# Performance work log

Hardware: AMD Instinct MI355X
Metric: run time of the kernel (lower is better)

The kernel has to match this reference:

```python
import jax, jax.numpy as jnp
import numpy as np


def conv1x1(x, w, b):
    # x: [B,C,H,W], w: [O,C], b: [O]
    return jnp.einsum('bchw,oc->bohw', x, w) + b[None, :, None, None]


def resize_bilinear(x, h, w):
    # matches torch F.interpolate(mode='bilinear', align_corners=False), no antialias
    B, C = x.shape[:2]
    return jax.image.resize(x, (B, C, h, w), method='bilinear', antialias=False)


def attend(q_map, k_map, v_map, num_heads, scale):
    # q_map/k_map/v_map: [B, hidden, H, W] -> out [B, hidden, H, W]
    B, D, H, W = q_map.shape
    hd = D // num_heads
    N = H * W
    q = q_map.reshape(B, num_heads, hd, N).transpose(0, 1, 3, 2)  # [B,h,N,d]
    k = k_map.reshape(B, num_heads, hd, N)                         # [B,h,d,N]
    v = v_map.reshape(B, num_heads, hd, N).transpose(0, 1, 3, 2)  # [B,h,N,d]
    scores = jnp.einsum('bhnd,bhdm->bhnm', q, k) * scale
    attn = jax.nn.softmax(scores, axis=-1)
    out = jnp.einsum('bhnm,bhmd->bhnd', attn, v)                   # [B,h,N,d]
    return out.transpose(0, 1, 3, 2).reshape(B, D, H, W)


NUM_HEADS = 8
HIDDEN = 256
HEAD_DIM = HIDDEN // NUM_HEADS
SCALE = HEAD_DIM ** -0.5


def setup_inputs() -> dict:
    key = jax.random.key(0)
    ks = jax.random.split(key, 20)
    C_h, C_l = 128, 256
    inp = {
        'high_feat': jax.random.normal(ks[0], (2, C_h, 64, 64), jnp.float32),
        'low_feat': jax.random.normal(ks[1], (2, C_l, 32, 32), jnp.float32),
    }
    def lin(k, o, c):
        kw, kb = jax.random.split(k)
        s = 1.0 / np.sqrt(c)
        return (jax.random.uniform(kw, (o, c), jnp.float32, -s, s),
                jax.random.uniform(kb, (o,), jnp.float32, -s, s))
    inp['q_high_w'], inp['q_high_b'] = lin(ks[2], HIDDEN, C_h)
    inp['k_high_w'], inp['k_high_b'] = lin(ks[3], HIDDEN, C_h)
    inp['v_high_w'], inp['v_high_b'] = lin(ks[4], HIDDEN, C_h)
    inp['q_low_w'], inp['q_low_b'] = lin(ks[5], HIDDEN, C_l)
    inp['k_low_w'], inp['k_low_b'] = lin(ks[6], HIDDEN, C_l)
    inp['v_low_w'], inp['v_low_b'] = lin(ks[7], HIDDEN, C_l)
    inp['out_high_w'], inp['out_high_b'] = lin(ks[8], C_h, HIDDEN)
    inp['out_low_w'], inp['out_low_b'] = lin(ks[9], C_l, HIDDEN)
    return inp


def reference(high_feat, low_feat,
              q_high_w, q_high_b, k_high_w, k_high_b, v_high_w, v_high_b,
              q_low_w, q_low_b, k_low_w, k_low_b, v_low_w, v_low_b,
              out_high_w, out_high_b, out_low_w, out_low_b):
    B, C_h, H, W = high_feat.shape
    _, C_l, Hl, Wl = low_feat.shape

    # high queries attend to upsampled-low keys/values
    low_up = resize_bilinear(low_feat, H, W)
    q_h = conv1x1(high_feat, q_high_w, q_high_b)
    k_l = conv1x1(low_up, k_low_w, k_low_b)
    v_l = conv1x1(low_up, v_low_w, v_low_b)
    high_out = attend(q_h, k_l, v_l, NUM_HEADS, SCALE)
    high_out = conv1x1(high_out, out_high_w, out_high_b)

    # low queries attend to downsampled-high keys/values
    q_l = conv1x1(low_feat, q_low_w, q_low_b)
    k_h = resize_bilinear(conv1x1(high_feat, k_high_w, k_high_b), Hl, Wl)
    v_h = resize_bilinear(conv1x1(high_feat, v_high_w, v_high_b), Hl, Wl)
    low_out = attend(q_l, k_h, v_h, NUM_HEADS, SCALE)
    low_out = conv1x1(low_out, out_low_w, out_low_b)

    return (high_out, low_out)
```

## Files before the change

### kernel.cpp

```cpp
#include <hip/hip_runtime.h>
#include <hip/hip_bf16.h>

#define HEADS 8
#define HD    32

typedef __attribute__((ext_vector_type(8))) short short8;
typedef __attribute__((ext_vector_type(4))) float f32x4;
typedef unsigned short us;

__device__ __forceinline__ us f2bf(float f) {
  union { __hip_bfloat16 h; us u; } cv;
  cv.h = __float2bfloat16(f);
  return cv.u;
}
__device__ __forceinline__ float bf2f(us u) {
  union { float f; unsigned int i; } cv;
  cv.i = ((unsigned int)u) << 16;
  return cv.f;
}
__device__ __forceinline__ float exp2_native(float x) {
  float r;
  asm("v_exp_f32 %0, %1" : "=v"(r) : "v"(x));
  return r;
}
__device__ __forceinline__ void glds16(const us* g, us* l) {
  __builtin_amdgcn_global_load_lds(
      (const __attribute__((address_space(1))) void*)g,
      (__attribute__((address_space(3))) void*)l, 16, 0, 0);
}

struct GP {
  const void* X; const float* W; const float* bias; void* out;
  int C, O, N, omode; float alpha;
};

template<int XMODE>
__global__ __launch_bounds__(256) void gemm_conv(
    GP g0, GP g1, GP g2, GP g3, int nb0, int nb1, int nb2) {
  __shared__ __align__(16) us Wh[2][64 * 32], Wl[2][64 * 32];
  __shared__ __align__(16) us Xh[2][64 * 32], Xl[2][64 * 32];
  int bid = blockIdx.x;
  GP g;
  if (bid < nb0) g = g0;
  else if (bid < nb0 + nb1) { g = g1; bid -= nb0; }
  else if (bid < nb0 + nb1 + nb2) { g = g2; bid -= nb0 + nb1; }
  else { g = g3; bid -= nb0 + nb1 + nb2; }
  const int C = g.C, O = g.O, N = g.N;
  int nx = N >> 6, nyo = O >> 6;
  int b = bid / (nx * nyo);
  int rr = bid - b * (nx * nyo);
  int o0 = (rr / nx) << 6;
  int n0 = (rr - (rr / nx) * nx) << 6;

  int tid = threadIdx.x, w = tid >> 6, l = tid & 63, lq = l & 15, l4 = l >> 4;

  int wr = tid >> 2, wcb = tid & 3;
  int xn = tid & 63, xcg = tid >> 6;
  const float* Wp = g.W + (size_t)(o0 + wr) * C + wcb * 8;
  const float* Xf = (const float*)g.X;
  const unsigned int* Xp = (const unsigned int*)g.X;
  size_t xbase = (size_t)b * C * N + n0 + xn;
  int wof = wr * 32 + ((wcb ^ ((wr >> 1) & 3)) << 3);
  int xof = xn * 32 + ((xcg ^ ((xn >> 1) & 3)) << 3);

  auto stage = [&](int s, int bufi) {
    int c0 = s << 5;
    float4 wa = *(const float4*)(Wp + c0);
    float4 wb = *(const float4*)(Wp + c0 + 4);
    float wv[8] = {wa.x, wa.y, wa.z, wa.w, wb.x, wb.y, wb.z, wb.w};
    short8 whv, wlv;
#pragma unroll
    for (int j = 0; j < 8; ++j) {
      us h = f2bf(wv[j]);
      whv[j] = (short)h;
      wlv[j] = (short)f2bf(wv[j] - bf2f(h));
    }
    *(short8*)&Wh[bufi][wof] = whv;
    *(short8*)&Wl[bufi][wof] = wlv;
    short8 xhv, xlv;
#pragma unroll
    for (int j = 0; j < 8; ++j) {
      int c = c0 + xcg * 8 + j;
      if constexpr (XMODE == 0) {
        float xv = Xf[xbase + (size_t)c * N];
        us h = f2bf(xv);
        xhv[j] = (short)h;
        xlv[j] = (short)f2bf(xv - bf2f(h));
      } else {
        unsigned int xv = Xp[xbase + (size_t)c * N];
        xhv[j] = (short)(xv >> 16);
        xlv[j] = (short)(xv & 0xffffu);
      }
    }
    *(short8*)&Xh[bufi][xof] = xhv;
    *(short8*)&Xl[bufi][xof] = xlv;
  };

  f32x4 acc[4] = {{0,0,0,0},{0,0,0,0},{0,0,0,0},{0,0,0,0}};
  int ns = C >> 5, cur = 0;
  stage(0, 0);
  for (int s = 0; s < ns; ++s) {
    __syncthreads();
    if (s + 1 < ns) stage(s + 1, cur ^ 1);
    int swz = (l4 ^ ((lq >> 1) & 3)) << 3;
    int arow = w * 16 + lq;
    short8 ah = *(const short8*)&Wh[cur][arow * 32 + swz];
    short8 al = *(const short8*)&Wl[cur][arow * 32 + swz];
    __builtin_amdgcn_s_setprio(1);
#pragma unroll
    for (int nf = 0; nf < 4; ++nf) {
      int brow = nf * 16 + lq;
      short8 bh = *(const short8*)&Xh[cur][brow * 32 + swz];
      short8 bl = *(const short8*)&Xl[cur][brow * 32 + swz];
      acc[nf] = __builtin_amdgcn_mfma_f32_16x16x32_bf16(ah, bh, acc[nf], 0, 0, 0);
      acc[nf] = __builtin_amdgcn_mfma_f32_16x16x32_bf16(ah, bl, acc[nf], 0, 0, 0);
      acc[nf] = __builtin_amdgcn_mfma_f32_16x16x32_bf16(al, bh, acc[nf], 0, 0, 0);
    }
    __builtin_amdgcn_s_setprio(0);
    cur ^= 1;
  }

  float bv[4];
#pragma unroll
  for (int r = 0; r < 4; ++r) bv[r] = g.bias[o0 + w * 16 + l4 * 4 + r];
  if (g.omode == 0) {
    us* ob = (us*)g.out;
#pragma unroll
    for (int nf = 0; nf < 4; ++nf) {
      ushort4 pk;
      pk.x = f2bf((acc[nf][0] + bv[0]) * g.alpha);
      pk.y = f2bf((acc[nf][1] + bv[1]) * g.alpha);
      pk.z = f2bf((acc[nf][2] + bv[2]) * g.alpha);
      pk.w = f2bf((acc[nf][3] + bv[3]) * g.alpha);
      *(ushort4*)&ob[((size_t)b * N + n0 + nf * 16 + lq) * O + o0 + w * 16 + l4 * 4] = pk;
    }
  } else if (g.omode == 1) {
    us* ob = (us*)g.out;
#pragma unroll
    for (int nf = 0; nf < 4; ++nf)
#pragma unroll
      for (int r = 0; r < 4; ++r)
        ob[((size_t)(b * O + o0 + w * 16 + l4 * 4 + r)) * N + n0 + nf * 16 + lq] =
            f2bf(acc[nf][r] + bv[r]);
  } else {
    float* of = (float*)g.out;
#pragma unroll
    for (int nf = 0; nf < 4; ++nf)
#pragma unroll
      for (int r = 0; r < 4; ++r)
        of[((size_t)(b * O + o0 + w * 16 + l4 * 4 + r)) * N + n0 + nf * 16 + lq] =
            acc[nf][r] + bv[r];
  }
}

__global__ __launch_bounds__(256) void upsample_both(
    const us* __restrict__ inT, us* __restrict__ outT,
    const us* __restrict__ inC, us* __restrict__ outC, int nbT, int BC) {
  if ((int)blockIdx.x < nbT) {
    int rowg = blockIdx.x * 4 + (threadIdx.x >> 6);
    int ch = (threadIdx.x & 63) * 4;
    int b = rowg >> 12, n = rowg & 4095;
    int y = n >> 6, x = n & 63;
    float sy = y * 0.5f - 0.25f, sx = x * 0.5f - 0.25f;
    int y0 = (int)floorf(sy), x0 = (int)floorf(sx);
    float fy = sy - (float)y0, fx = sx - (float)x0;
    int y0c = max(y0, 0), y1c = min(y0 + 1, 31);
    int x0c = max(x0, 0), x1c = min(x0 + 1, 31);
    const us* ip = inT + (size_t)b * 1024 * 256 + ch;
    ushort4 v00 = *(const ushort4*)&ip[(size_t)(y0c * 32 + x0c) * 256];
    ushort4 v01 = *(const ushort4*)&ip[(size_t)(y0c * 32 + x1c) * 256];
    ushort4 v10 = *(const ushort4*)&ip[(size_t)(y1c * 32 + x0c) * 256];
    ushort4 v11 = *(const ushort4*)&ip[(size_t)(y1c * 32 + x1c) * 256];
    float w00 = (1.f - fy) * (1.f - fx), w01 = (1.f - fy) * fx;
    float w10 = fy * (1.f - fx), w11 = fy * fx;
    ushort4 o;
    o.x = f2bf(w00 * bf2f(v00.x) + w01 * bf2f(v01.x) + w10 * bf2f(v10.x) + w11 * bf2f(v11.x));
    o.y = f2bf(w00 * bf2f(v00.y) + w01 * bf2f(v01.y) + w10 * bf2f(v10.y) + w11 * bf2f(v11.y));
    o.z = f2bf(w00 * bf2f(v00.z) + w01 * bf2f(v01.z) + w10 * bf2f(v10.z) + w11 * bf2f(v11.z));
    o.w = f2bf(w00 * bf2f(v00.w) + w01 * bf2f(v01.w) + w10 * bf2f(v10.w) + w11 * bf2f(v11.w));
    *(ushort4*)&outT[((size_t)b * 4096 + n) * 256 + ch] = o;
  } else {
    int t = ((int)blockIdx.x - nbT) * 256 + threadIdx.x;
    if (t >= BC * 64) return;
    int y = t & 63, bc = t >> 6;
    float sy = y * 0.5f - 0.25f;
    int y0 = (int)floorf(sy);
    float fy = sy - (float)y0;
    int y0c = max(y0, 0), y1c = min(y0 + 1, 31);
    const us* r0 = inC + (size_t)bc * 1024 + y0c * 32;
    const us* r1 = inC + (size_t)bc * 1024 + y1c * 32;
    float m[32];
#pragma unroll
    for (int j = 0; j < 32; j += 8) {
      short8 a = *(const short8*)(r0 + j);
      short8 c = *(const short8*)(r1 + j);
#pragma unroll
      for (int e = 0; e < 8; ++e)
        m[j + e] = (1.f - fy) * bf2f((us)a[e]) + fy * bf2f((us)c[e]);
    }
    us* op = outC + (size_t)bc * 4096 + y * 64;
    short8 o8;
#pragma unroll
    for (int xo = 0; xo < 64; ++xo) {
      int k = xo >> 1;
      float v;
      if (xo & 1) v = (k < 31) ? 0.75f * m[k] + 0.25f * m[k + 1] : m[31];
      else        v = (k > 0) ? 0.25f * m[k - 1] + 0.75f * m[k] : m[0];
      o8[xo & 7] = (short)f2bf(v);
      if ((xo & 7) == 7) *(short8*)(op + (xo & ~7)) = o8;
    }
  }
}

__global__ __launch_bounds__(256) void downsample_pack_k(
    const float* __restrict__ in, unsigned int* __restrict__ opk, int BC) {
  int t = blockIdx.x * 256 + threadIdx.x;
  if (t >= BC * 1024) return;
  int x = t & 31, y = (t >> 5) & 31, bc = t >> 10;
  const float* ip = in + (size_t)bc * 4096 + (y * 2) * 64 + x * 2;
  float v = 0.25f * (ip[0] + ip[1] + ip[64] + ip[65]);
  us h = f2bf(v);
  opk[t] = ((unsigned int)h << 16) | f2bf(v - bf2f(h));
}

__global__ __launch_bounds__(256) void attn_mfma(
    const us* __restrict__ qT0, const us* __restrict__ kT0,
    const us* __restrict__ vC0, unsigned int* __restrict__ o0,
    int N0, int nb0,
    const us* __restrict__ qT1, const us* __restrict__ kT1,
    const us* __restrict__ vC1, unsigned int* __restrict__ o1,
    int N1) {
  __shared__ __align__(16) us Kt[2][64 * 32];
  __shared__ __align__(16) us Vt[2][32 * 64];
  __shared__ __align__(16) us Pt[8][16 * 64];

  int bid = blockIdx.x;
  const us *qT, *kT, *vC; unsigned int* opk; int N, bh, qb;
  if (bid < nb0) {
    qT = qT0; kT = kT0; vC = vC0; opk = o0; N = N0;
    int xcd = bid & 7, slot = bid >> 3, nqb = N0 >> 7;
    qb = slot & (nqb - 1);
    bh = ((slot / nqb) << 3) | xcd;
  } else {
    bid -= nb0;
    qT = qT1; kT = kT1; vC = vC1; opk = o1; N = N1;
    int xcd = bid & 7, slot = bid >> 3, nqb = N1 >> 7;
    qb = slot & (nqb - 1);
    bh = ((slot / nqb) << 3) | xcd;
  }
  int b = bh >> 3, h = bh & 7;
  int tid = threadIdx.x;
  int w = tid >> 6, l = tid & 63;
  int lq = l & 15, l4 = l >> 4;

  short8 qfrag[2];
#pragma unroll
  for (int g = 0; g < 2; ++g) {
    const us* qp = qT + ((size_t)(b * N + qb * 128 + g * 64 + w * 16 + lq)) * 256 +
                   h * 32 + l4 * 8;
    qfrag[g] = *(const short8*)qp;
  }

  int rK = w * 16 + (l >> 2);
  const us* gK = kT + ((size_t)(b * N + rK)) * 256 + h * 32 +
                 (((l & 3) ^ ((rK >> 1) & 3)) << 3);
  int dV = w * 8 + (l >> 3);
  const us* gV = vC + ((size_t)(b * 256 + h * 32 + dV)) * N +
                 (((l & 7) ^ (dV & 7)) << 3);

  f32x4 acc0[2] = {{0,0,0,0},{0,0,0,0}};
  f32x4 acc1[2] = {{0,0,0,0},{0,0,0,0}};
  f32x4 acc2[2] = {{0,0,0,0},{0,0,0,0}};
  short8 ones;
#pragma unroll
  for (int j = 0; j < 8; ++j) ones[j] = (short)0x3F80;

  glds16(gK, &Kt[0][w * 512]);
  glds16(gV, &Vt[0][w * 512]);

  int nt = N >> 6, cur = 0;
  for (int t = 0; t < nt; ++t) {
    __syncthreads();
    if (t + 1 < nt) {
      glds16(gK + (size_t)(t + 1) * 64 * 256, &Kt[cur ^ 1][w * 512]);
      glds16(gV + (t + 1) * 64, &Vt[cur ^ 1][w * 512]);
    }
    const us* Kb = Kt[cur];
    const us* Vb = Vt[cur];

#pragma unroll
    for (int kg = 0; kg < 4; ++kg) {
      int key = kg * 16 + lq;
      short8 a = *(const short8*)&Kb[key * 32 + ((l4 ^ ((key >> 1) & 3)) << 3)];
      f32x4 zero = {0.f, 0.f, 0.f, 0.f};
      int key0 = kg * 16 + l4 * 4;
      int pof = lq * 64 + (((key0 >> 3) ^ (lq & 7)) << 3) + (key0 & 7);
#pragma unroll
      for (int g = 0; g < 2; ++g) {
        __builtin_amdgcn_s_setprio(1);
        f32x4 s = __builtin_amdgcn_mfma_f32_16x16x32_bf16(a, qfrag[g], zero, 0, 0, 0);
        __builtin_amdgcn_s_setprio(0);
        float p0 = exp2_native(s[0]);
        float p1 = exp2_native(s[1]);
        float p2 = exp2_native(s[2]);
        float p3 = exp2_native(s[3]);
        unsigned int r01, r23;
        asm("v_cvt_pk_bf16_f32 %0, %1, %2" : "=v"(r01) : "v"(p0), "v"(p1));
        asm("v_cvt_pk_bf16_f32 %0, %1, %2" : "=v"(r23) : "v"(p2), "v"(p3));
        uint2 pk; pk.x = r01; pk.y = r23;
        *(uint2*)&Pt[w * 2 + g][pof] = pk;
      }
    }

#pragma unroll
    for (int kh = 0; kh < 2; ++kh) {
      int d0 = lq, d1 = 16 + lq;
      short8 vf0 = *(const short8*)&Vb[d0 * 64 + (((kh * 4 + l4) ^ (d0 & 7)) << 3)];
      short8 vf1 = *(const short8*)&Vb[d1 * 64 + (((kh * 4 + l4) ^ (d1 & 7)) << 3)];
      int pof = lq * 64 + (((kh * 4 + l4) ^ (lq & 7)) << 3);
#pragma unroll
      for (int g = 0; g < 2; ++g) {
        short8 pfr = *(const short8*)&Pt[w * 2 + g][pof];
        __builtin_amdgcn_s_setprio(1);
        acc0[g] = __builtin_amdgcn_mfma_f32_16x16x32_bf16(vf0, pfr, acc0[g], 0, 0, 0);
        acc1[g] = __builtin_amdgcn_mfma_f32_16x16x32_bf16(vf1, pfr, acc1[g], 0, 0, 0);
        acc2[g] = __builtin_amdgcn_mfma_f32_16x16x32_bf16(ones, pfr, acc2[g], 0, 0, 0);
        __builtin_amdgcn_s_setprio(0);
      }
    }
    cur ^= 1;
  }

#pragma unroll
  for (int g = 0; g < 2; ++g) {
    float inv = 1.f / acc2[g][0];
    unsigned int* op = opk + ((size_t)(b * 256 + h * 32)) * N +
                       qb * 128 + g * 64 + w * 16 + lq;
#pragma unroll
    for (int r = 0; r < 4; ++r) {
      float v0 = acc0[g][r] * inv;
      us h0 = f2bf(v0);
      op[(size_t)(l4 * 4 + r) * N] = ((unsigned int)h0 << 16) | f2bf(v0 - bf2f(h0));
      float v1 = acc1[g][r] * inv;
      us h1 = f2bf(v1);
      op[(size_t)(16 + l4 * 4 + r) * N] = ((unsigned int)h1 << 16) | f2bf(v1 - bf2f(h1));
    }
  }
}

extern "C" void kernel_launch(void* const* d_in, const int* in_sizes, int n_in,
                              void* d_out, int out_size, void* d_ws, size_t ws_size,
                              hipStream_t stream) {
  const float* high_feat  = (const float*)d_in[0];
  const float* low_feat   = (const float*)d_in[1];
  const float* q_high_w   = (const float*)d_in[2];
  const float* q_high_b   = (const float*)d_in[3];
  const float* k_high_w   = (const float*)d_in[4];
  const float* k_high_b   = (const float*)d_in[5];
  const float* v_high_w   = (const float*)d_in[6];
  const float* v_high_b   = (const float*)d_in[7];
  const float* q_low_w    = (const float*)d_in[8];
  const float* q_low_b    = (const float*)d_in[9];
  const float* k_low_w    = (const float*)d_in[10];
  const float* k_low_b    = (const float*)d_in[11];
  const float* v_low_w    = (const float*)d_in[12];
  const float* v_low_b    = (const float*)d_in[13];
  const float* out_high_w = (const float*)d_in[14];
  const float* out_high_b = (const float*)d_in[15];
  const float* out_low_w  = (const float*)d_in[16];
  const float* out_low_b  = (const float*)d_in[17];

  const int B = 2, Nh = 4096, Nl = 1024;
  const float qa = 0.17677669529663689f * 1.4426950408889634f;

  char* p = (char*)d_ws;
  us* qT    = (us*)p; p += (size_t)2 * 4096 * 256 * 2;
  us* kTb   = (us*)p; p += (size_t)2 * 4096 * 256 * 2;
  us* vCb   = (us*)p; p += (size_t)2 * 256 * 4096 * 2;
  us* klbT  = (us*)p; p += (size_t)2 * 1024 * 256 * 2;
  us* vlb   = (us*)p; p += (size_t)2 * 256 * 1024 * 2;
  unsigned int* aoh  = (unsigned int*)p; p += (size_t)2 * 256 * 4096 * 4;
  unsigned int* hfdn = (unsigned int*)p; p += (size_t)2 * 128 * 1024 * 4;
  us* qTl   = (us*)p; p += (size_t)2 * 1024 * 256 * 2;
  us* kTl   = (us*)p; p += (size_t)2 * 1024 * 256 * 2;
  us* vCl   = (us*)p; p += (size_t)2 * 256 * 1024 * 2;
  unsigned int* aol  = (unsigned int*)p; p += (size_t)2 * 256 * 1024 * 4;

  float* out_high = (float*)d_out;
  float* out_low  = out_high + 2 * 128 * 4096;

  downsample_pack_k<<<(B * 128 * 1024) / 256, 256, 0, stream>>>(high_feat, hfdn, B * 128);

  {
    GP s0 = {low_feat,  k_low_w,  k_low_b,  klbT, 256, 256, Nl, 0, 1.0f};
    GP s1 = {low_feat,  v_low_w,  v_low_b,  vlb,  256, 256, Nl, 1, 1.0f};
    GP s2 = {high_feat, q_high_w, q_high_b, qT,   128, 256, Nh, 0, qa};
    GP s3 = {low_feat,  q_low_w,  q_low_b,  qTl,  256, 256, Nl, 0, qa};
    gemm_conv<0><<<896, 256, 0, stream>>>(s0, s1, s2, s3, 128, 128, 512);
  }
  upsample_both<<<2048 + 128, 256, 0, stream>>>(klbT, kTb, vlb, vCb, 2048, B * 256);
  {
    GP s0 = {hfdn, k_high_w, k_high_b, kTl, 128, 256, Nl, 0, 1.0f};
    GP s1 = {hfdn, v_high_w, v_high_b, vCl, 128, 256, Nl, 1, 1.0f};
    gemm_conv<1><<<256, 256, 0, stream>>>(s0, s1, s0, s0, 128, 128, 0);
  }
  attn_mfma<<<16 * (Nh / 128) + 16 * (Nl / 128), 256, 0, stream>>>(
      qT, kTb, vCb, aoh, Nh, 16 * (Nh / 128),
      qTl, kTl, vCl, aol, Nl);
  {
    GP s0 = {aoh, out_high_w, out_high_b, out_high, 256, 128, Nh, 2, 1.0f};
    GP s1 = {aol, out_low_w,  out_low_b,  out_low,  256, 256, Nl, 2, 1.0f};
    gemm_conv<1><<<384, 256, 0, stream>>>(s0, s1, s0, s0, 256, 128, 0);
  }
}
```

Measured before the change: 125.6 us.

## Split attention key range in two and add a partial-sum reduce kernel

The attention kernel now splits each query block's key/value range into two halves handled by separate workgroups, doubling the grid. Each half writes unnormalised fp32 numerators and denominators to workspace. A new reduce kernel sums the two halves, normalises, and packs the bf16 hi/lo output as before. This aims at better CU utilisation and load balance across the long high-resolution blocks. The cost is an extra launch, fp32 partial buffers that are written and read back, and a duplicated Q load per split.

```diff
diff --git a/kernel.cpp b/kernel.cpp
--- a/kernel.cpp
+++ b/kernel.cpp
@@ -225,30 +225,33 @@
 
 __global__ __launch_bounds__(256) void attn_mfma(
     const us* __restrict__ qT0, const us* __restrict__ kT0,
-    const us* __restrict__ vC0, unsigned int* __restrict__ o0,
+    const us* __restrict__ vC0, float* __restrict__ pn0, float* __restrict__ pd0,
     int N0, int nb0,
     const us* __restrict__ qT1, const us* __restrict__ kT1,
-    const us* __restrict__ vC1, unsigned int* __restrict__ o1,
+    const us* __restrict__ vC1, float* __restrict__ pn1, float* __restrict__ pd1,
     int N1) {
   __shared__ __align__(16) us Kt[2][64 * 32];
   __shared__ __align__(16) us Vt[2][32 * 64];
   __shared__ __align__(16) us Pt[8][16 * 64];
 
   int bid = blockIdx.x;
-  const us *qT, *kT, *vC; unsigned int* opk; int N, bh, qb;
+  const us *qT, *kT, *vC; float *pn, *pd; int N, bh, qb, sp;
   if (bid < nb0) {
-    qT = qT0; kT = kT0; vC = vC0; opk = o0; N = N0;
-    int xcd = bid & 7, slot = bid >> 3, nqb = N0 >> 7;
-    qb = slot & (nqb - 1);
-    bh = ((slot / nqb) << 3) | xcd;
+    qT = qT0; kT = kT0; vC = vC0; pn = pn0; pd = pd0; N = N0;
+    int xcd = bid & 7, slot = bid >> 3, nqb2 = (N0 >> 7) * 2;
+    int qs = slot % nqb2;
+    bh = ((slot / nqb2) << 3) | xcd;
+    qb = qs >> 1; sp = qs & 1;
   } else {
     bid -= nb0;
-    qT = qT1; kT = kT1; vC = vC1; opk = o1; N = N1;
-    int xcd = bid & 7, slot = bid >> 3, nqb = N1 >> 7;
-    qb = slot & (nqb - 1);
-    bh = ((slot / nqb) << 3) | xcd;
+    qT = qT1; kT = kT1; vC = vC1; pn = pn1; pd = pd1; N = N1;
+    int xcd = bid & 7, slot = bid >> 3, nqb2 = (N1 >> 7) * 2;
+    int qs = slot % nqb2;
+    bh = ((slot / nqb2) << 3) | xcd;
+    qb = qs >> 1; sp = qs & 1;
   }
   int b = bh >> 3, h = bh & 7;
+  int SK = N >> 1;
   int tid = threadIdx.x;
   int w = tid >> 6, l = tid & 63;
   int lq = l & 15, l4 = l >> 4;
@@ -262,10 +265,10 @@
   }
 
   int rK = w * 16 + (l >> 2);
-  const us* gK = kT + ((size_t)(b * N + rK)) * 256 + h * 32 +
+  const us* gK = kT + ((size_t)(b * N + sp * SK + rK)) * 256 + h * 32 +
                  (((l & 3) ^ ((rK >> 1) & 3)) << 3);
   int dV = w * 8 + (l >> 3);
-  const us* gV = vC + ((size_t)(b * 256 + h * 32 + dV)) * N +
+  const us* gV = vC + ((size_t)(b * 256 + h * 32 + dV)) * N + sp * SK +
                  (((l & 7) ^ (dV & 7)) << 3);
 
   f32x4 acc0[2] = {{0,0,0,0},{0,0,0,0}};
@@ -278,7 +281,7 @@
   glds16(gK, &Kt[0][w * 512]);
   glds16(gV, &Vt[0][w * 512]);
 
-  int nt = N >> 6, cur = 0;
+  int nt = SK >> 6, cur = 0;
   for (int t = 0; t < nt; ++t) {
     __syncthreads();
     if (t + 1 < nt) {
@@ -331,20 +334,43 @@
     cur ^= 1;
   }
 
+  size_t nbase = ((size_t)((sp * 2 + b) * 8 + h)) * 32 * N;
+  size_t dbase = ((size_t)((sp * 2 + b) * 8 + h)) * N;
 #pragma unroll
   for (int g = 0; g < 2; ++g) {
-    float inv = 1.f / acc2[g][0];
-    unsigned int* op = opk + ((size_t)(b * 256 + h * 32)) * N +
-                       qb * 128 + g * 64 + w * 16 + lq;
+    int q = qb * 128 + g * 64 + w * 16 + lq;
 #pragma unroll
     for (int r = 0; r < 4; ++r) {
-      float v0 = acc0[g][r] * inv;
-      us h0 = f2bf(v0);
-      op[(size_t)(l4 * 4 + r) * N] = ((unsigned int)h0 << 16) | f2bf(v0 - bf2f(h0));
-      float v1 = acc1[g][r] * inv;
-      us h1 = f2bf(v1);
-      op[(size_t)(16 + l4 * 4 + r) * N] = ((unsigned int)h1 << 16) | f2bf(v1 - bf2f(h1));
-    }
+      pn[nbase + (size_t)(l4 * 4 + r) * N + q] = acc0[g][r];
+      pn[nbase + (size_t)(16 + l4 * 4 + r) * N + q] = acc1[g][r];
+    }
+    if (l4 == 0) pd[dbase + q] = acc2[g][0];
+  }
+}
+
+__global__ __launch_bounds__(256) void attn_reduce(
+    const float* __restrict__ pnH, const float* __restrict__ pdH,
+    unsigned int* __restrict__ oH, int NH, int nb0,
+    const float* __restrict__ pnL, const float* __restrict__ pdL,
+    unsigned int* __restrict__ oL, int NL) {
+  int bid = blockIdx.x;
+  const float *pn, *pd; unsigned int* opk; int N;
+  if (bid < nb0) { pn = pnH; pd = pdH; opk = oH; N = NH; }
+  else { bid -= nb0; pn = pnL; pd = pdL; opk = oL; N = NL; }
+  int t = bid * 256 + threadIdx.x;
+  int bh = t / N, q = t - bh * N;
+  int b = bh >> 3, h = bh & 7;
+  size_t S = (size_t)16 * 32 * N;
+  size_t Sd = (size_t)16 * N;
+  size_t nb = ((size_t)bh) * 32 * N + q;
+  float den = pd[(size_t)bh * N + q] + pd[Sd + (size_t)bh * N + q];
+  float inv = 1.f / den;
+  unsigned int* op = opk + ((size_t)(b * 256 + h * 32)) * N + q;
+#pragma unroll
+  for (int d = 0; d < 32; ++d) {
+    float v = (pn[nb + (size_t)d * N] + pn[S + nb + (size_t)d * N]) * inv;
+    us hh = f2bf(v);
+    op[(size_t)d * N] = ((unsigned int)hh << 16) | f2bf(v - bf2f(hh));
   }
 }
 
@@ -385,6 +411,10 @@
   us* kTl   = (us*)p; p += (size_t)2 * 1024 * 256 * 2;
   us* vCl   = (us*)p; p += (size_t)2 * 256 * 1024 * 2;
   unsigned int* aol  = (unsigned int*)p; p += (size_t)2 * 256 * 1024 * 4;
+  float* pnH = (float*)p; p += (size_t)2 * 16 * 32 * 4096 * 4;
+  float* pdH = (float*)p; p += (size_t)2 * 16 * 4096 * 4;
+  float* pnL = (float*)p; p += (size_t)2 * 16 * 32 * 1024 * 4;
+  float* pdL = (float*)p; p += (size_t)2 * 16 * 1024 * 4;
 
   float* out_high = (float*)d_out;
   float* out_low  = out_high + 2 * 128 * 4096;
@@ -404,9 +434,14 @@
     GP s1 = {hfdn, v_high_w, v_high_b, vCl, 128, 256, Nl, 1, 1.0f};
     gemm_conv<1><<<256, 256, 0, stream>>>(s0, s1, s0, s0, 128, 128, 0);
   }
-  attn_mfma<<<16 * (Nh / 128) + 16 * (Nl / 128), 256, 0, stream>>>(
-      qT, kTb, vCb, aoh, Nh, 16 * (Nh / 128),
-      qTl, kTl, vCl, aol, Nl);
+  {
+    int nb0 = 16 * (Nh / 128) * 2, nb1 = 16 * (Nl / 128) * 2;
+    attn_mfma<<<nb0 + nb1, 256, 0, stream>>>(
+        qT, kTb, vCb, pnH, pdH, Nh, nb0,
+        qTl, kTl, vCl, pnL, pdL, Nl);
+    attn_reduce<<<(16 * Nh) / 256 + (16 * Nl) / 256, 256, 0, stream>>>(
+        pnH, pdH, aoh, Nh, (16 * Nh) / 256, pnL, pdL, aol, Nl);
+  }
   {
     GP s0 = {aoh, out_high_w, out_high_b, out_high, 256, 128, Nh, 2, 1.0f};
     GP s1 = {aol, out_low_w,  out_low_b,  out_low,  256, 256, Nl, 2, 1.0f};
```

Result: faster. 115.6 us (-8.0%).
